# Performance work log

Hardware: AMD Instinct MI355X
Metric: run time of the kernel (lower is better)

Reference implementation:

```python
import jax, jax.numpy as jnp
import numpy as np

N_NODES = 50000
N_EDGES = 1000000
H_DIM = 128
OUT_DIM = 64
N_RELS = 16  # num_bases == num_rels


def setup_inputs() -> dict:
    key = jax.random.key(0)
    ks = jax.random.split(key, 12)
    node_ids = jnp.arange(N_NODES, dtype=jnp.int64) if jax.config.jax_enable_x64 else jnp.arange(N_NODES, dtype=jnp.int32)
    src = jax.random.randint(ks[0], (N_EDGES,), 0, N_NODES)
    dst = jax.random.randint(ks[1], (N_EDGES,), 0, N_NODES)
    etype = jax.random.randint(ks[2], (N_EDGES,), 0, N_RELS)
    norm = jax.random.uniform(ks[3], (N_EDGES, 1), dtype=jnp.float32)
    s1 = 1.0 / np.sqrt(H_DIM)
    s2 = 1.0 / np.sqrt(OUT_DIM)
    emb = jax.random.normal(ks[4], (N_NODES, H_DIM), dtype=jnp.float32)
    V1 = jax.random.normal(ks[5], (N_RELS, H_DIM, H_DIM), dtype=jnp.float32) * s1
    comp1 = jax.random.normal(ks[6], (N_RELS, N_RELS), dtype=jnp.float32) * (1.0 / np.sqrt(N_RELS))
    bias1 = jnp.zeros((H_DIM,), dtype=jnp.float32)
    V2 = jax.random.normal(ks[7], (N_RELS, H_DIM, OUT_DIM), dtype=jnp.float32) * s2
    comp2 = jax.random.normal(ks[8], (N_RELS, N_RELS), dtype=jnp.float32) * (1.0 / np.sqrt(N_RELS))
    bias2 = jnp.zeros((OUT_DIM,), dtype=jnp.float32)
    return {"node_ids": node_ids, "src": src, "dst": dst, "etype": etype, "norm": norm,
            "emb": emb, "V1": V1, "comp1": comp1, "bias1": bias1,
            "V2": V2, "comp2": comp2, "bias2": bias2}


def _rel_graph_conv(x, src, dst, etype, norm, V, comp, bias, num_nodes):
    # Basis decomposition: W_r = sum_b comp[r, b] * V_b  -> [R, in, out]
    W = jnp.einsum('rb,bio->rio', comp, V)
    # Per-relation transform of all nodes: [R, N, out]
    Y = jnp.einsum('ni,rio->rno', x, W)
    # Per-edge message: gather (etype, src) then scale by norm  -> [E, out]
    m = Y[etype, src] * norm
    # Scatter-add to destination nodes
    h = jax.ops.segment_sum(m, dst, num_segments=num_nodes)
    return h + bias


def reference(node_ids, src, dst, etype, norm, emb, V1, comp1, bias1, V2, comp2, bias2):
    x = emb[node_ids]  # [N, H]
    h = jax.nn.relu(_rel_graph_conv(x, src, dst, etype, norm, V1, comp1, bias1, x.shape[0]))
    h = _rel_graph_conv(h, src, dst, etype, norm, V2, comp2, bias2, x.shape[0])
    return h
```

## Files before the change

kernel.cpp:

```cpp
#include <hip/hip_runtime.h>
#include <hip/hip_bf16.h>


typedef short bf16x8 __attribute__((ext_vector_type(8)));
typedef float f32x4 __attribute__((ext_vector_type(4)));

#define RELS 16
#define HDIM 128
#define DSTBLK 64
#define MT_P 4
#define CHUNK 32

__device__ inline unsigned short f2bf(float f) {
  unsigned int u = __float_as_uint(f);
  unsigned int r = u + 0x7FFFu + ((u >> 16) & 1u);
  return (unsigned short)(r >> 16);
}

__device__ __forceinline__ unsigned pk_bf16(float a, float b) {
  __hip_bfloat162 p = __float22bfloat162_rn(make_float2(a, b));
  return *(unsigned*)&p;
}

__global__ void prep_fused(const float* __restrict__ emb, unsigned short* __restrict__ embh,
                           int n8,
                           const float* __restrict__ comp1, const float* __restrict__ V1,
                           const float* __restrict__ comp2, const float* __restrict__ V2,
                           unsigned short* __restrict__ W1t, unsigned short* __restrict__ W2t) {
  int idx = blockIdx.x * blockDim.x + threadIdx.x;
  if (idx < n8) {
    float4 a = ((const float4*)emb)[idx * 2];
    float4 b = ((const float4*)emb)[idx * 2 + 1];
    uint4 o;
    o.x = pk_bf16(a.x, a.y);
    o.y = pk_bf16(a.z, a.w);
    o.z = pk_bf16(b.x, b.y);
    o.w = pk_bf16(b.z, b.w);
    ((uint4*)embh)[idx] = o;
    return;
  }
  int j = idx - n8;
  const int PER_R = HDIM * (HDIM + 64);
  if (j >= RELS * PER_R) return;
  int r = j / PER_R;
  int rem = j - r * PER_R;
  if (rem < HDIM * HDIM) {
    int o = rem >> 7, k = rem & 127;
    float s = 0.f;
#pragma unroll
    for (int b = 0; b < RELS; b++)
      s = fmaf(comp1[r * RELS + b], V1[(size_t)b * HDIM * HDIM + (size_t)k * HDIM + o], s);
    W1t[(size_t)r * HDIM * HDIM + rem] = f2bf(s);
  } else {
    int rr = rem - HDIM * HDIM;
    int o = rr >> 7, k = rr & 127;
    float s = 0.f;
#pragma unroll
    for (int b = 0; b < RELS; b++)
      s = fmaf(comp2[r * RELS + b], V2[(size_t)b * HDIM * 64 + (size_t)k * 64 + o], s);
    W2t[(size_t)r * 64 * HDIM + rr] = f2bf(s);
  }
}

__global__ void hist_bins(const int* __restrict__ dst, const int* __restrict__ etype,
                          int n, int* __restrict__ counts) {
  for (int i = blockIdx.x * blockDim.x + threadIdx.x; i < n; i += gridDim.x * blockDim.x)
    atomicAdd(&counts[(dst[i] >> 6) * RELS + etype[i]], 1);
}

__global__ void scan_offsets(const int* __restrict__ counts, int* __restrict__ offsets, int nbins) {
  __shared__ int csum[256];
  const int t = threadIdx.x;
  const int CH = (nbins + 255) / 256;
  int lo = t * CH, hi = min(lo + CH, nbins);
  int s = 0;
  for (int i = lo; i < hi; i++) s += (counts[i] + 15) & ~15;
  csum[t] = s;
  __syncthreads();
#pragma unroll
  for (int d = 1; d < 256; d <<= 1) {
    int v = (t >= d) ? csum[t - d] : 0;
    __syncthreads();
    csum[t] += v;
    __syncthreads();
  }
  int run = (t == 0) ? 0 : csum[t - 1];
  for (int i = lo; i < hi; i++) {
    offsets[i] = run;
    run += (counts[i] + 15) & ~15;
  }
  if (lo < nbins && hi == nbins) offsets[nbins] = run;
}

__global__ void scatter_bins(const int* __restrict__ src, const int* __restrict__ dst,
                             const int* __restrict__ etype, const float* __restrict__ norm,
                             int n, const int* __restrict__ offsets, int* __restrict__ cursor,
                             uint2* __restrict__ ebuf) {
  for (int i = blockIdx.x * blockDim.x + threadIdx.x; i < n; i += gridDim.x * blockDim.x) {
    int d = dst[i];
    int b = (d >> 6) * RELS + etype[i];
    int p = offsets[b] + atomicAdd(&cursor[b], 1);
    ebuf[p] = make_uint2((unsigned)src[i] | ((unsigned)(d & 63) << 20),
                         (unsigned)f2bf(norm[i]));
  }
}

template <int OUT, bool BF16_RELU_OUT>
__launch_bounds__(256, 3)
__global__ void rgcn_layer(const unsigned short* __restrict__ Xb,
                           const unsigned short* __restrict__ Wt,
                           const uint2* __restrict__ ebuf,
                           const int* __restrict__ offsets, const int* __restrict__ counts,
                           const float* __restrict__ bias, void* __restrict__ Hout,
                           int nNodes) {
  constexpr int NT = OUT / 64;
  __shared__ __align__(16) unsigned short xs[2][CHUNK][136];
  __shared__ __align__(16) unsigned short ys[OUT][40];
  __shared__ __align__(16) unsigned short pmat[2][DSTBLK][40];

  const int t = threadIdx.x;
  const int w = t >> 6;
  const int lane = t & 63;
  const int quad = lane >> 4;
  const int l16 = lane & 15;
  const int r0 = t >> 4;
  const int k8 = t & 15;
  const bool isHandler = (t & 7) == 0;
  const int myCol = t >> 3;
  const int nodeBase = blockIdx.x * DSTBLK;
  const int binBase = blockIdx.x * RELS;
  const int colBase = w * (OUT / 4);

  for (int i = t; i < 2 * CHUNK * 136 / 8; i += 256) ((uint4*)xs)[i] = make_uint4(0, 0, 0, 0);
  for (int i = t; i < OUT * 40 / 8; i += 256) ((uint4*)ys)[i] = make_uint4(0, 0, 0, 0);
  for (int i = t; i < 2 * DSTBLK * 40 / 8; i += 256) ((uint4*)pmat)[i] = make_uint4(0, 0, 0, 0);

  f32x4 pacc[MT_P][NT] = {};

  int bin = 0, base = 0, binEnd = 0, realEnd = 0;
  for (; bin < RELS; bin++) {
    base = offsets[binBase + bin];
    binEnd = offsets[binBase + bin + 1];
    if (base < binEnd) { realEnd = base + counts[binBase + bin]; break; }
  }

  __syncthreads();

  int pdA = -1, pdB = -1;
  if (bin < RELS) {
    int nR = min(CHUNK, realEnd - base);
    if (r0 < nR) {
      uint2 e = ebuf[base + r0];
      *(uint4*)&xs[0][r0][k8 * 8] = *(const uint4*)(Xb + (size_t)(e.x & 0xFFFFFu) * HDIM + k8 * 8);
    }
    if (16 + r0 < nR) {
      uint2 e = ebuf[base + 16 + r0];
      *(uint4*)&xs[0][16 + r0][k8 * 8] = *(const uint4*)(Xb + (size_t)(e.x & 0xFFFFFu) * HDIM + k8 * 8);
    }
    if (isHandler && myCol < nR) {
      uint2 m = ebuf[base + myCol];
      int dl = (int)(m.x >> 20) & 63;
      pmat[0][dl][myCol] = (unsigned short)(m.y & 0xFFFFu);
      pdB = dl;
    }
  }
  __syncthreads();

  int cb = 0;
  int curRel = -1;
  bf16x8 wf[4][NT];

  while (bin < RELS) {
    const int nRows = min(CHUNK, realEnd - base);

    if (bin != curRel) {
      curRel = bin;
      const unsigned short* Wr = Wt + (size_t)bin * OUT * HDIM;
#pragma unroll
      for (int ks = 0; ks < 4; ks++)
#pragma unroll
        for (int nt = 0; nt < NT; nt++)
          wf[ks][nt] = *(const bf16x8*)(Wr + (size_t)(colBase + nt * 16 + l16) * HDIM + ks * 32 + quad * 8);
    }

    int nbin = bin, nbase = base + CHUNK, nbinEnd = binEnd, nrealEnd = realEnd;
    if (nbase >= binEnd) {
      for (nbin = bin + 1; nbin < RELS; nbin++) {
        nbase = offsets[binBase + nbin];
        nbinEnd = offsets[binBase + nbin + 1];
        if (nbase < nbinEnd) { nrealEnd = nbase + counts[binBase + nbin]; break; }
      }
    }
    const bool hasNext = nbin < RELS;
    const int nR = hasNext ? min(CHUNK, nrealEnd - nbase) : 0;

    uint2 e0, e1, em;
    if (hasNext) {
      if (r0 < nR) e0 = ebuf[nbase + r0];
      if (16 + r0 < nR) e1 = ebuf[nbase + 16 + r0];
      if (isHandler && myCol < nR) em = ebuf[nbase + myCol];
    }

#pragma unroll
    for (int mt = 0; mt < 2; mt++) {
      if (mt * 16 < nRows) {
        f32x4 dacc[NT] = {};
#pragma unroll
        for (int ks = 0; ks < 4; ks++) {
          bf16x8 a = *(const bf16x8*)&xs[cb][mt * 16 + l16][ks * 32 + quad * 8];
#pragma unroll
          for (int nt = 0; nt < NT; nt++)
            dacc[nt] = __builtin_amdgcn_mfma_f32_16x16x32_bf16(a, wf[ks][nt], dacc[nt], 0, 0, 0);
        }
#pragma unroll
        for (int nt = 0; nt < NT; nt++) {
          uint2 pk;
          pk.x = pk_bf16(dacc[nt][0], dacc[nt][1]);
          pk.y = pk_bf16(dacc[nt][2], dacc[nt][3]);
          *(uint2*)&ys[colBase + nt * 16 + l16][mt * 16 + quad * 4] = pk;
        }
      }
    }

    uint4 g0, g1;
    if (hasNext) {
      if (r0 < nR) g0 = *(const uint4*)(Xb + (size_t)(e0.x & 0xFFFFFu) * HDIM + k8 * 8);
      if (16 + r0 < nR) g1 = *(const uint4*)(Xb + (size_t)(e1.x & 0xFFFFFu) * HDIM + k8 * 8);
    }

    {
      bf16x8 bfv[NT];
#pragma unroll
      for (int nt = 0; nt < NT; nt++)
        bfv[nt] = *(const bf16x8*)&ys[colBase + nt * 16 + l16][quad * 8];
#pragma unroll
      for (int mt = 0; mt < MT_P; mt++) {
        bf16x8 a = *(const bf16x8*)&pmat[cb][mt * 16 + l16][quad * 8];
#pragma unroll
        for (int nt = 0; nt < NT; nt++)
          pacc[mt][nt] = __builtin_amdgcn_mfma_f32_16x16x32_bf16(a, bfv[nt], pacc[mt][nt], 0, 0, 0);
      }
    }

    if (hasNext) {
      if (r0 < nR) *(uint4*)&xs[cb ^ 1][r0][k8 * 8] = g0;
      if (16 + r0 < nR) *(uint4*)&xs[cb ^ 1][16 + r0][k8 * 8] = g1;
      if (isHandler) {
        if (pdA >= 0) pmat[cb ^ 1][pdA][myCol] = 0;
        if (myCol < nR) {
          int dl = (int)(em.x >> 20) & 63;
          pmat[cb ^ 1][dl][myCol] = (unsigned short)(em.y & 0xFFFFu);
          pdA = dl;
        } else {
          pdA = -1;
        }
      }
    }
    { int tmp = pdA; pdA = pdB; pdB = tmp; }

    if (hasNext) __syncthreads();

    bin = nbin; base = nbase; binEnd = nbinEnd; realEnd = nrealEnd;
    cb ^= 1;
  }

#pragma unroll
  for (int mt = 0; mt < MT_P; mt++) {
#pragma unroll
    for (int reg = 0; reg < 4; reg++) {
      int node = nodeBase + mt * 16 + quad * 4 + reg;
      if (node < nNodes) {
#pragma unroll
        for (int nt = 0; nt < NT; nt++) {
          int col = colBase + nt * 16 + l16;
          float v = pacc[mt][nt][reg] + bias[col];
          if constexpr (BF16_RELU_OUT)
            ((unsigned short*)Hout)[(size_t)node * OUT + col] = f2bf(fmaxf(v, 0.f));
          else
            ((float*)Hout)[(size_t)node * OUT + col] = v;
        }
      }
    }
  }
}

extern "C" void kernel_launch(void* const* d_in, const int* in_sizes, int n_in,
                              void* d_out, int out_size, void* d_ws, size_t ws_size,
                              hipStream_t stream) {
  const int*   src   = (const int*)d_in[1];
  const int*   dst   = (const int*)d_in[2];
  const int*   etype = (const int*)d_in[3];
  const float* norm  = (const float*)d_in[4];
  const float* emb   = (const float*)d_in[5];
  const float* V1    = (const float*)d_in[6];
  const float* comp1 = (const float*)d_in[7];
  const float* bias1 = (const float*)d_in[8];
  const float* V2    = (const float*)d_in[9];
  const float* comp2 = (const float*)d_in[10];
  const float* bias2 = (const float*)d_in[11];
  float* out = (float*)d_out;

  const int N = in_sizes[0];
  const int E = in_sizes[1];
  const int H = 128, O = 64;
  const int NB = (N + DSTBLK - 1) / DSTBLK;
  const int NBINS = NB * RELS;
  const int EPAD_MAX = E + NBINS * 16 + 64;

  char* ws = (char*)d_ws;
  size_t off = 0;
  auto alloc = [&](size_t bytes) -> void* {
    void* p = ws + off;
    off += (bytes + 255) & ~(size_t)255;
    return p;
  };
  unsigned short* W1t  = (unsigned short*)alloc(sizeof(short) * RELS * H * H);
  unsigned short* W2t  = (unsigned short*)alloc(sizeof(short) * RELS * O * H);
  unsigned short* embh = (unsigned short*)alloc(sizeof(short) * (size_t)N * H);
  unsigned short* h1b  = (unsigned short*)alloc(sizeof(short) * (size_t)N * H);
  uint2* ebuf = (uint2*)alloc(sizeof(uint2) * EPAD_MAX);
  int* cc      = (int*)alloc(sizeof(int) * 2 * NBINS);
  int* counts  = cc;
  int* cursor  = cc + NBINS;
  int* offsets = (int*)alloc(sizeof(int) * (NBINS + 1));

  hipMemsetAsync(cc, 0, sizeof(int) * 2 * NBINS, stream);

  const int n8 = N * H / 8;
  prep_fused<<<(n8 + RELS * H * (H + O) + 255) / 256, 256, 0, stream>>>(
      emb, embh, n8, comp1, V1, comp2, V2, W1t, W2t);
  hist_bins<<<512, 256, 0, stream>>>(dst, etype, E, counts);
  scan_offsets<<<1, 256, 0, stream>>>(counts, offsets, NBINS);
  scatter_bins<<<1024, 256, 0, stream>>>(src, dst, etype, norm, E, offsets, cursor, ebuf);

  rgcn_layer<128, true><<<NB, 256, 0, stream>>>(embh, W1t, ebuf, offsets, counts, bias1, (void*)h1b, N);
  rgcn_layer<64, false><<<NB, 256, 0, stream>>>(h1b, W2t, ebuf, offsets, counts, bias2, (void*)out, N);
}
```

Before: 505.2 us.

## Deepen the edge pipeline, resize destination blocks to 66, and use an LDS histogram

The layer kernel now fetches edge descriptors two chunks ahead. It issues the next chunk's feature gathers and the next relation's weight loads earlier, so their latency overlaps the MFMA work. The destination block size changes from 64 to 66 nodes, with a fifth padded MFMA row tile. The likely aim is to cut the block count so the whole grid fits in one occupancy wave, at the cost of some wasted MFMA rows. The bin histogram now accumulates in shared memory before global atomics, which reduces contention on global atomics.

```diff
diff --git a/kernel.cpp b/kernel.cpp
--- a/kernel.cpp
+++ b/kernel.cpp
@@ -7,9 +7,10 @@
 
 #define RELS 16
 #define HDIM 128
-#define DSTBLK 64
-#define MT_P 4
+#define DSTBLK 66
+#define MT_P 5
 #define CHUNK 32
+#define MAXBINS 12288
 
 __device__ inline unsigned short f2bf(float f) {
   unsigned int u = __float_as_uint(f);
@@ -63,9 +64,17 @@
 }
 
 __global__ void hist_bins(const int* __restrict__ dst, const int* __restrict__ etype,
-                          int n, int* __restrict__ counts) {
+                          int n, int nbins, int* __restrict__ counts) {
+  __shared__ int lh[MAXBINS];
+  for (int j = threadIdx.x; j < nbins; j += blockDim.x) lh[j] = 0;
+  __syncthreads();
   for (int i = blockIdx.x * blockDim.x + threadIdx.x; i < n; i += gridDim.x * blockDim.x)
-    atomicAdd(&counts[(dst[i] >> 6) * RELS + etype[i]], 1);
+    atomicAdd(&lh[(dst[i] / DSTBLK) * RELS + etype[i]], 1);
+  __syncthreads();
+  for (int j = threadIdx.x; j < nbins; j += blockDim.x) {
+    int c = lh[j];
+    if (c) atomicAdd(&counts[j], c);
+  }
 }
 
 __global__ void scan_offsets(const int* __restrict__ counts, int* __restrict__ offsets, int nbins) {
@@ -98,9 +107,10 @@
                              uint2* __restrict__ ebuf) {
   for (int i = blockIdx.x * blockDim.x + threadIdx.x; i < n; i += gridDim.x * blockDim.x) {
     int d = dst[i];
-    int b = (d >> 6) * RELS + etype[i];
+    int blk = d / DSTBLK;
+    int b = blk * RELS + etype[i];
     int p = offsets[b] + atomicAdd(&cursor[b], 1);
-    ebuf[p] = make_uint2((unsigned)src[i] | ((unsigned)(d & 63) << 20),
+    ebuf[p] = make_uint2((unsigned)src[i] | ((unsigned)(d - blk * DSTBLK) << 20),
                          (unsigned)f2bf(norm[i]));
   }
 }
@@ -116,7 +126,7 @@
   constexpr int NT = OUT / 64;
   __shared__ __align__(16) unsigned short xs[2][CHUNK][136];
   __shared__ __align__(16) unsigned short ys[OUT][40];
-  __shared__ __align__(16) unsigned short pmat[2][DSTBLK][40];
+  __shared__ __align__(16) unsigned short pmat[2][80][40];
 
   const int t = threadIdx.x;
   const int w = t >> 6;
@@ -133,72 +143,74 @@
 
   for (int i = t; i < 2 * CHUNK * 136 / 8; i += 256) ((uint4*)xs)[i] = make_uint4(0, 0, 0, 0);
   for (int i = t; i < OUT * 40 / 8; i += 256) ((uint4*)ys)[i] = make_uint4(0, 0, 0, 0);
-  for (int i = t; i < 2 * DSTBLK * 40 / 8; i += 256) ((uint4*)pmat)[i] = make_uint4(0, 0, 0, 0);
+  for (int i = t; i < 2 * 80 * 40 / 8; i += 256) ((uint4*)pmat)[i] = make_uint4(0, 0, 0, 0);
 
   f32x4 pacc[MT_P][NT] = {};
 
-  int bin = 0, base = 0, binEnd = 0, realEnd = 0;
-  for (; bin < RELS; bin++) {
-    base = offsets[binBase + bin];
-    binEnd = offsets[binBase + bin + 1];
-    if (base < binEnd) { realEnd = base + counts[binBase + bin]; break; }
+  int cBin = 0, cBase = 0, cBinEnd = 0, cRealEnd = 0;
+  for (; cBin < RELS; cBin++) {
+    cBase = offsets[binBase + cBin];
+    cBinEnd = offsets[binBase + cBin + 1];
+    if (cBase < cBinEnd) { cRealEnd = cBase + counts[binBase + cBin]; break; }
+  }
+  int nBin = cBin, nBase = cBase + CHUNK, nBinEnd = cBinEnd, nRealEnd = cRealEnd;
+  if (cBin < RELS && nBase >= cBinEnd) {
+    for (nBin = cBin + 1; nBin < RELS; nBin++) {
+      nBase = offsets[binBase + nBin];
+      nBinEnd = offsets[binBase + nBin + 1];
+      if (nBase < nBinEnd) { nRealEnd = nBase + counts[binBase + nBin]; break; }
+    }
   }
 
   __syncthreads();
 
   int pdA = -1, pdB = -1;
-  if (bin < RELS) {
-    int nR = min(CHUNK, realEnd - base);
+  uint2 eC0, eC1, eCm;
+  if (cBin < RELS) {
+    int nR = min(CHUNK, cRealEnd - cBase);
     if (r0 < nR) {
-      uint2 e = ebuf[base + r0];
+      uint2 e = ebuf[cBase + r0];
       *(uint4*)&xs[0][r0][k8 * 8] = *(const uint4*)(Xb + (size_t)(e.x & 0xFFFFFu) * HDIM + k8 * 8);
     }
     if (16 + r0 < nR) {
-      uint2 e = ebuf[base + 16 + r0];
+      uint2 e = ebuf[cBase + 16 + r0];
       *(uint4*)&xs[0][16 + r0][k8 * 8] = *(const uint4*)(Xb + (size_t)(e.x & 0xFFFFFu) * HDIM + k8 * 8);
     }
     if (isHandler && myCol < nR) {
-      uint2 m = ebuf[base + myCol];
-      int dl = (int)(m.x >> 20) & 63;
+      uint2 m = ebuf[cBase + myCol];
+      int dl = (int)(m.x >> 20) & 127;
       pmat[0][dl][myCol] = (unsigned short)(m.y & 0xFFFFu);
       pdB = dl;
     }
+    if (nBin < RELS) {
+      int nR1 = min(CHUNK, nRealEnd - nBase);
+      if (r0 < nR1) eC0 = ebuf[nBase + r0];
+      if (16 + r0 < nR1) eC1 = ebuf[nBase + 16 + r0];
+      if (isHandler && myCol < nR1) eCm = ebuf[nBase + myCol];
+    }
+  }
+
+  bf16x8 wf[4][NT];
+  if (cBin < RELS) {
+    const unsigned short* Wr = Wt + (size_t)cBin * OUT * HDIM;
+#pragma unroll
+    for (int ks = 0; ks < 4; ks++)
+#pragma unroll
+      for (int nt = 0; nt < NT; nt++)
+        wf[ks][nt] = *(const bf16x8*)(Wr + (size_t)(colBase + nt * 16 + l16) * HDIM + ks * 32 + quad * 8);
   }
   __syncthreads();
 
   int cb = 0;
-  int curRel = -1;
-  bf16x8 wf[4][NT];
-
-  while (bin < RELS) {
-    const int nRows = min(CHUNK, realEnd - base);
-
-    if (bin != curRel) {
-      curRel = bin;
-      const unsigned short* Wr = Wt + (size_t)bin * OUT * HDIM;
-#pragma unroll
-      for (int ks = 0; ks < 4; ks++)
-#pragma unroll
-        for (int nt = 0; nt < NT; nt++)
-          wf[ks][nt] = *(const bf16x8*)(Wr + (size_t)(colBase + nt * 16 + l16) * HDIM + ks * 32 + quad * 8);
-    }
-
-    int nbin = bin, nbase = base + CHUNK, nbinEnd = binEnd, nrealEnd = realEnd;
-    if (nbase >= binEnd) {
-      for (nbin = bin + 1; nbin < RELS; nbin++) {
-        nbase = offsets[binBase + nbin];
-        nbinEnd = offsets[binBase + nbin + 1];
-        if (nbase < nbinEnd) { nrealEnd = nbase + counts[binBase + nbin]; break; }
-      }
-    }
-    const bool hasNext = nbin < RELS;
-    const int nR = hasNext ? min(CHUNK, nrealEnd - nbase) : 0;
-
-    uint2 e0, e1, em;
+  while (cBin < RELS) {
+    const int nRows = min(CHUNK, cRealEnd - cBase);
+    const bool hasNext = nBin < RELS;
+    const int nR1 = hasNext ? min(CHUNK, nRealEnd - nBase) : 0;
+
+    uint4 g0, g1;
     if (hasNext) {
-      if (r0 < nR) e0 = ebuf[nbase + r0];
-      if (16 + r0 < nR) e1 = ebuf[nbase + 16 + r0];
-      if (isHandler && myCol < nR) em = ebuf[nbase + myCol];
+      if (r0 < nR1) g0 = *(const uint4*)(Xb + (size_t)(eC0.x & 0xFFFFFu) * HDIM + k8 * 8);
+      if (16 + r0 < nR1) g1 = *(const uint4*)(Xb + (size_t)(eC1.x & 0xFFFFFu) * HDIM + k8 * 8);
     }
 
 #pragma unroll
@@ -222,10 +234,29 @@
       }
     }
 
-    uint4 g0, g1;
-    if (hasNext) {
-      if (r0 < nR) g0 = *(const uint4*)(Xb + (size_t)(e0.x & 0xFFFFFu) * HDIM + k8 * 8);
-      if (16 + r0 < nR) g1 = *(const uint4*)(Xb + (size_t)(e1.x & 0xFFFFFu) * HDIM + k8 * 8);
+    if (hasNext && nBin != cBin) {
+      const unsigned short* Wr = Wt + (size_t)nBin * OUT * HDIM;
+#pragma unroll
+      for (int ks = 0; ks < 4; ks++)
+#pragma unroll
+        for (int nt = 0; nt < NT; nt++)
+          wf[ks][nt] = *(const bf16x8*)(Wr + (size_t)(colBase + nt * 16 + l16) * HDIM + ks * 32 + quad * 8);
+    }
+
+    int n2Bin = nBin, n2Base = nBase + CHUNK, n2BinEnd = nBinEnd, n2RealEnd = nRealEnd;
+    if (hasNext && n2Base >= nBinEnd) {
+      for (n2Bin = nBin + 1; n2Bin < RELS; n2Bin++) {
+        n2Base = offsets[binBase + n2Bin];
+        n2BinEnd = offsets[binBase + n2Bin + 1];
+        if (n2Base < n2BinEnd) { n2RealEnd = n2Base + counts[binBase + n2Bin]; break; }
+      }
+    }
+    uint2 en0, en1, enm;
+    if (hasNext && n2Bin < RELS) {
+      int nR2 = min(CHUNK, n2RealEnd - n2Base);
+      if (r0 < nR2) en0 = ebuf[n2Base + r0];
+      if (16 + r0 < nR2) en1 = ebuf[n2Base + 16 + r0];
+      if (isHandler && myCol < nR2) enm = ebuf[n2Base + myCol];
     }
 
     {
@@ -243,13 +274,13 @@
     }
 
     if (hasNext) {
-      if (r0 < nR) *(uint4*)&xs[cb ^ 1][r0][k8 * 8] = g0;
-      if (16 + r0 < nR) *(uint4*)&xs[cb ^ 1][16 + r0][k8 * 8] = g1;
+      if (r0 < nR1) *(uint4*)&xs[cb ^ 1][r0][k8 * 8] = g0;
+      if (16 + r0 < nR1) *(uint4*)&xs[cb ^ 1][16 + r0][k8 * 8] = g1;
       if (isHandler) {
         if (pdA >= 0) pmat[cb ^ 1][pdA][myCol] = 0;
-        if (myCol < nR) {
-          int dl = (int)(em.x >> 20) & 63;
-          pmat[cb ^ 1][dl][myCol] = (unsigned short)(em.y & 0xFFFFu);
+        if (myCol < nR1) {
+          int dl = (int)(eCm.x >> 20) & 127;
+          pmat[cb ^ 1][dl][myCol] = (unsigned short)(eCm.y & 0xFFFFu);
           pdA = dl;
         } else {
           pdA = -1;
@@ -260,7 +291,9 @@
 
     if (hasNext) __syncthreads();
 
-    bin = nbin; base = nbase; binEnd = nbinEnd; realEnd = nrealEnd;
+    cBin = nBin; cBase = nBase; cBinEnd = nBinEnd; cRealEnd = nRealEnd;
+    nBin = n2Bin; nBase = n2Base; nBinEnd = n2BinEnd; nRealEnd = n2RealEnd;
+    eC0 = en0; eC1 = en1; eCm = enm;
     cb ^= 1;
   }
 
@@ -268,8 +301,9 @@
   for (int mt = 0; mt < MT_P; mt++) {
 #pragma unroll
     for (int reg = 0; reg < 4; reg++) {
-      int node = nodeBase + mt * 16 + quad * 4 + reg;
-      if (node < nNodes) {
+      int ld = mt * 16 + quad * 4 + reg;
+      int node = nodeBase + ld;
+      if (ld < DSTBLK && node < nNodes) {
 #pragma unroll
         for (int nt = 0; nt < NT; nt++) {
           int col = colBase + nt * 16 + l16;
@@ -329,7 +363,7 @@
   const int n8 = N * H / 8;
   prep_fused<<<(n8 + RELS * H * (H + O) + 255) / 256, 256, 0, stream>>>(
       emb, embh, n8, comp1, V1, comp2, V2, W1t, W2t);
-  hist_bins<<<512, 256, 0, stream>>>(dst, etype, E, counts);
+  hist_bins<<<256, 256, 0, stream>>>(dst, etype, E, NBINS, counts);
   scan_offsets<<<1, 256, 0, stream>>>(counts, offsets, NBINS);
   scatter_bins<<<1024, 256, 0, stream>>>(src, dst, etype, norm, E, offsets, cursor, ebuf);
 
```

Result: faster. 462.5 us (-8.5%).
